# Kernel optimization log

Hardware: AMD Instinct MI355X
Metric: run time of the kernel (lower is better)

The kernel has to match this reference:

```python
import jax, jax.numpy as jnp
import numpy as np

B, T, D, H = 8, 4096, 256, 256

def setup_inputs() -> dict:
    key = jax.random.key(0)
    ks = jax.random.split(key, 6)
    scale = 1.0 / np.sqrt(D)
    return {
        "x": jax.random.normal(ks[0], (B, T, D), dtype=jnp.float32),
        "h0": jax.random.normal(ks[1], (B, H), dtype=jnp.float32),
        "Wz": jax.random.normal(ks[2], (H, D), dtype=jnp.float32) * scale,
        "bz": jax.random.normal(ks[3], (H,), dtype=jnp.float32) * scale,
        "Wh": jax.random.normal(ks[4], (H, D), dtype=jnp.float32) * scale,
        "bh": jax.random.normal(ks[5], (H,), dtype=jnp.float32) * scale,
    }

def reference(x, h0, Wz, bz, Wh, bh):
    # gate and update depend only on the input (minGRU): compute in one shot
    gate = jax.nn.sigmoid(jnp.einsum("btd,hd->bth", x, Wz) + bz)   # [B,T,H]
    update = jnp.einsum("btd,hd->bth", x, Wh) + bh                  # [B,T,H]

    def step(h, gu):
        g, u = gu
        h_new = (1.0 - g) * h + g * u
        return h_new, h_new

    # scan over time; xs laid out [T,B,H]
    _, hs = jax.lax.scan(step, h0, (jnp.swapaxes(gate, 0, 1), jnp.swapaxes(update, 0, 1)))
    return jnp.swapaxes(hs, 0, 1)  # [B,T,H]
```

## Files before the change

### kernel.cpp

```cpp
#include <hip/hip_runtime.h>
#include <hip/hip_fp16.h>


namespace {
constexpr int kB  = 8;
constexpr int kT  = 4096;
constexpr int kD  = 256;
constexpr int kH  = 256;
constexpr int kBT = kB * kT;

constexpr int TM  = 128;
constexpr int TH  = 64;
constexpr int BK  = 64;
constexpr int kNT = kT / TM;
constexpr int kNChain = kB * (kH / TH);
constexpr int EPS = 66;
}

typedef short s16x8 __attribute__((ext_vector_type(8)));
typedef short s16x4 __attribute__((ext_vector_type(4)));
typedef float f32x4 __attribute__((ext_vector_type(4)));

__device__ __forceinline__ short f2bf(float f) {
    union { float f; unsigned int u; } v; v.f = f;
    unsigned int r = v.u + 0x7fffu + ((v.u >> 16) & 1u);
    return (short)(r >> 16);
}

__device__ __forceinline__ unsigned int cvt_pk_bf16(float lo, float hi) {
    unsigned int r;
    asm("v_cvt_pk_bf16_f32 %0, %1, %2" : "=v"(r) : "v"(lo), "v"(hi));
    return r;
}

__device__ __forceinline__ void load_lds16(const void* g, void* l) {
    __builtin_amdgcn_global_load_lds(
        (const __attribute__((address_space(1))) void*)g,
        (__attribute__((address_space(3))) void*)l, 16, 0, 0);
}

__global__ __launch_bounds__(256)
void prep(const float* __restrict__ Wz,
          const float* __restrict__ Wh,
          unsigned short* __restrict__ wzb,
          unsigned short* __restrict__ whb,
          float4* __restrict__ aggz)
{
    constexpr int W4 = kH * kD / 4;
    const int i = blockIdx.x * 256 + threadIdx.x;

    if (i >= 2 * W4) {
        float4 z; z.x = 0.f; z.y = 0.f; z.z = 0.f; z.w = 0.f;
        aggz[i - 2 * W4] = z;
        return;
    }
    const float* src; unsigned short* dst; int j;
    if (i < W4) { src = Wz; dst = wzb; j = i; }
    else        { src = Wh; dst = whb; j = i - W4; }
    const float4 v = ((const float4*)src)[j];
    s16x4 p;
    p[0] = f2bf(v.x); p[1] = f2bf(v.y); p[2] = f2bf(v.z); p[3] = f2bf(v.w);
    ((s16x4*)dst)[j] = p;
}

__global__ __launch_bounds__(256, 4)
void gemm_scan_fused(const float* __restrict__ x,
                     const unsigned short* __restrict__ wzb,
                     const unsigned short* __restrict__ whb,
                     const float* __restrict__ bz,
                     const float* __restrict__ bh,
                     const float* __restrict__ h0,
                     unsigned long long* __restrict__ agg,
                     float* __restrict__ out)
{
    __shared__ __align__(16) unsigned char smem[36096];
    unsigned short* Xs  = (unsigned short*)smem;
    unsigned short* Wzs = Xs  + 128 * 64;
    unsigned short* Whs = Wzs + 64 * 64;
    __half* a_lds   = (__half*)smem;
    __half* b_lds   = a_lds + 128 * EPS;
    float2* sub_lds = (float2*)(smem + 33792);
    float*  hs_lds  = (float*)(smem + 35840);

    const int tid  = threadIdx.x;
    const int lane = tid & 63;
    const int wv   = tid >> 6;
    const int ln15 = lane & 15;
    const int quad = lane >> 4;
    const int wr0  = (wv & 1) * 64;
    const int wc0  = (wv >> 1) * 32;

    const int chain = blockIdx.x;
    const int t     = blockIdx.y;
    const int b     = chain >> 2;
    const int col0  = (chain & 3) * TH;
    const int row0  = b * kT + t * TM;

    const int srow = lane >> 3;
    const int swslot = (lane & 7) ^ srow;

    f32x4 accZ[4][2] = {};
    f32x4 accU[4][2] = {};

    for (int k0 = 0; k0 < kD; k0 += BK) {
        #pragma unroll
        for (int s = 0; s < 2; ++s) {
            const int seg = wv * 2 + s;
            const int m = seg * 8 + srow;
            load_lds16(wzb + (size_t)(col0 + m) * kD + k0 + swslot * 8,
                       Wzs + seg * 512);
            load_lds16(whb + (size_t)(col0 + m) * kD + k0 + swslot * 8,
                       Whs + seg * 512);
        }
        #pragma unroll
        for (int j = 0; j < 4; ++j) {
            const int bi  = j * 256 + tid;
            const int r   = bi >> 3;
            const int blk = bi & 7;
            const float* src = x + (size_t)(row0 + r) * kD + k0 + blk * 8;
            const float4 v0 = *(const float4*)src;
            const float4 v1 = *(const float4*)(src + 4);
            union { unsigned int u[4]; s16x8 v; } pk;
            pk.u[0] = cvt_pk_bf16(v0.x, v0.y);
            pk.u[1] = cvt_pk_bf16(v0.z, v0.w);
            pk.u[2] = cvt_pk_bf16(v1.x, v1.y);
            pk.u[3] = cvt_pk_bf16(v1.z, v1.w);
            *(s16x8*)&Xs[r * 64 + ((blk ^ (r & 7)) << 3)] = pk.v;
        }
        __syncthreads();

        #pragma unroll
        for (int kk = 0; kk < BK; kk += 32) {
            const int bblk = (kk >> 3) + quad;
            s16x8 af[4], bzf[2], buf[2];
            #pragma unroll
            for (int mt = 0; mt < 4; ++mt) {
                const int r = wr0 + mt * 16 + ln15;
                af[mt] = *(const s16x8*)&Xs[r * 64 + ((bblk ^ (r & 7)) << 3)];
            }
            #pragma unroll
            for (int nt = 0; nt < 2; ++nt) {
                const int rw = wc0 + nt * 16 + ln15;
                const int so = (bblk ^ (rw & 7)) << 3;
                bzf[nt] = *(const s16x8*)&Wzs[rw * 64 + so];
                buf[nt] = *(const s16x8*)&Whs[rw * 64 + so];
            }
            #pragma unroll
            for (int mt = 0; mt < 4; ++mt) {
                #pragma unroll
                for (int nt = 0; nt < 2; ++nt) {
                    accZ[mt][nt] = __builtin_amdgcn_mfma_f32_16x16x32_bf16(
                        af[mt], bzf[nt], accZ[mt][nt], 0, 0, 0);
                    accU[mt][nt] = __builtin_amdgcn_mfma_f32_16x16x32_bf16(
                        af[mt], buf[nt], accU[mt][nt], 0, 0, 0);
                }
            }
        }
        __syncthreads();
    }

    #pragma unroll
    for (int nt = 0; nt < 2; ++nt) {
        const int col = col0 + wc0 + nt * 16 + ln15;
        const int lc  = wc0 + nt * 16 + ln15;
        const float bzv = bz[col];
        const float bhv = bh[col];
        #pragma unroll
        for (int mt = 0; mt < 4; ++mt) {
            const int rb = wr0 + mt * 16 + quad * 4;
            #pragma unroll
            for (int r = 0; r < 4; ++r) {
                const float z = accZ[mt][nt][r] + bzv;
                const float g = 1.0f / (1.0f + __expf(-z));
                const float u = accU[mt][nt][r] + bhv;
                a_lds[(rb + r) * EPS + lc] = __float2half_rn(1.0f - g);
                b_lds[(rb + r) * EPS + lc] = __float2half_rn(g * u);
            }
        }
    }
    __syncthreads();

    const int s = tid >> 6;
    const int h = tid & 63;
    {
        float A = 1.0f, Bv = 0.0f;
        #pragma unroll 8
        for (int r = s * 32; r < s * 32 + 32; ++r) {
            const float a  = __half2float(a_lds[r * EPS + h]);
            const float bb = __half2float(b_lds[r * EPS + h]);
            Bv = fmaf(a, Bv, bb);
            A *= a;
        }
        float2 o; o.x = A; o.y = Bv;
        sub_lds[s * 64 + h] = o;
    }
    __syncthreads();

    if (tid < 64) {
        float A = 1.0f, Bv = 0.0f;
        #pragma unroll
        for (int s2 = 0; s2 < 4; ++s2) {
            const float2 g = sub_lds[s2 * 64 + tid];
            Bv = fmaf(g.x, Bv, g.y);
            A *= g.x;
        }
        union { float2 f; unsigned long long u; } pk;
        pk.f.x = A; pk.f.y = Bv;
        pk.u |= 1ull;
        __hip_atomic_store(&agg[(size_t)(chain * kNT + t) * 64 + tid], pk.u,
                           __ATOMIC_RELAXED, __HIP_MEMORY_SCOPE_AGENT);

        float hs = h0[(size_t)b * kH + col0 + tid];
        for (int j0 = 0; j0 < t; j0 += 8) {
            const int nb = (t - j0 < 8) ? (t - j0) : 8;
            unsigned long long u[8];
            #pragma unroll
            for (int q = 0; q < 8; ++q)
                if (q < nb)
                    u[q] = __hip_atomic_load(
                        &agg[(size_t)(chain * kNT + j0 + q) * 64 + tid],
                        __ATOMIC_RELAXED, __HIP_MEMORY_SCOPE_AGENT);
            #pragma unroll
            for (int q = 0; q < 8; ++q) {
                if (q < nb) {
                    while (u[q] == 0ull)
                        u[q] = __hip_atomic_load(
                            &agg[(size_t)(chain * kNT + j0 + q) * 64 + tid],
                            __ATOMIC_RELAXED, __HIP_MEMORY_SCOPE_AGENT);
                    union { unsigned long long u; float2 f; } qk; qk.u = u[q];
                    hs = fmaf(qk.f.x, hs, qk.f.y);
                }
            }
        }
        hs_lds[tid] = hs;
    }
    __syncthreads();

    {
        float hv = hs_lds[h];
        #pragma unroll
        for (int s2 = 0; s2 < s; ++s2) {
            const float2 g = sub_lds[s2 * 64 + h];
            hv = fmaf(g.x, hv, g.y);
        }
        #pragma unroll 8
        for (int r = 0; r < 32; ++r) {
            const int lr = s * 32 + r;
            const float a  = __half2float(a_lds[lr * EPS + h]);
            const float bb = __half2float(b_lds[lr * EPS + h]);
            hv = fmaf(a, hv, bb);
            __builtin_nontemporal_store(hv, &out[(size_t)(row0 + lr) * kH + col0 + h]);
        }
    }
}

extern "C" void kernel_launch(void* const* d_in, const int* in_sizes, int n_in,
                              void* d_out, int out_size, void* d_ws, size_t ws_size,
                              hipStream_t stream)
{
    const float* x  = (const float*)d_in[0];
    const float* h0 = (const float*)d_in[1];
    const float* Wz = (const float*)d_in[2];
    const float* bz = (const float*)d_in[3];
    const float* Wh = (const float*)d_in[4];
    const float* bh = (const float*)d_in[5];
    float* out = (float*)d_out;

    unsigned char* ws = (unsigned char*)d_ws;
    unsigned short* wzb = (unsigned short*)ws;   ws += (size_t)kH * kD * 2;
    unsigned short* whb = (unsigned short*)ws;   ws += (size_t)kH * kD * 2;
    unsigned long long* agg = (unsigned long long*)ws;

    constexpr int PREP_ITEMS = 2 * (kH * kD / 4)
                             + kNChain * kNT * TH * 8 / 16;
    prep<<<PREP_ITEMS / 256, 256, 0, stream>>>(
        Wz, Wh, wzb, whb, (float4*)agg);
    gemm_scan_fused<<<dim3(kNChain, kNT), 256, 0, stream>>>(
        x, wzb, whb, bz, bh, h0, agg, out);
}
```

Baseline: 116.0 us.

## Prefetch next x K-slice into registers during MFMA and raise MFMA wave priority

The GEMM K loop is restructured so the global loads of the next 64-wide x slice are issued into registers before the current slice's MFMAs run. The loaded values are converted to bf16 and written to LDS after the compute barrier, which hides global load latency behind matrix work. The MFMA block is also wrapped in s_setprio so waves doing math get issue priority. This costs extra VGPRs for the prefetch buffers, which may lower occupancy, and W loads still sit on the critical path between barriers.

```diff
diff --git a/kernel.cpp b/kernel.cpp
--- a/kernel.cpp
+++ b/kernel.cpp
@@ -99,35 +99,59 @@
     const int srow = lane >> 3;
     const int swslot = (lane & 7) ^ srow;
 
+    const int xr   = (tid >> 3) & 127;
+    float4 xv0[4], xv1[4];
+
     f32x4 accZ[4][2] = {};
     f32x4 accU[4][2] = {};
 
-    for (int k0 = 0; k0 < kD; k0 += BK) {
-        #pragma unroll
-        for (int s = 0; s < 2; ++s) {
-            const int seg = wv * 2 + s;
-            const int m = seg * 8 + srow;
-            load_lds16(wzb + (size_t)(col0 + m) * kD + k0 + swslot * 8,
-                       Wzs + seg * 512);
-            load_lds16(whb + (size_t)(col0 + m) * kD + k0 + swslot * 8,
-                       Whs + seg * 512);
-        }
-        #pragma unroll
-        for (int j = 0; j < 4; ++j) {
-            const int bi  = j * 256 + tid;
-            const int r   = bi >> 3;
-            const int blk = bi & 7;
-            const float* src = x + (size_t)(row0 + r) * kD + k0 + blk * 8;
-            const float4 v0 = *(const float4*)src;
-            const float4 v1 = *(const float4*)(src + 4);
-            union { unsigned int u[4]; s16x8 v; } pk;
-            pk.u[0] = cvt_pk_bf16(v0.x, v0.y);
-            pk.u[1] = cvt_pk_bf16(v0.z, v0.w);
-            pk.u[2] = cvt_pk_bf16(v1.x, v1.y);
-            pk.u[3] = cvt_pk_bf16(v1.z, v1.w);
-            *(s16x8*)&Xs[r * 64 + ((blk ^ (r & 7)) << 3)] = pk.v;
-        }
-        __syncthreads();
+    #pragma unroll
+    for (int j = 0; j < 4; ++j) {
+        const int bi  = j * 256 + tid;
+        const int r   = bi >> 3;
+        const int blk = bi & 7;
+        const float* src = x + (size_t)(row0 + r) * kD + blk * 8;
+        xv0[j] = *(const float4*)src;
+        xv1[j] = *(const float4*)(src + 4);
+    }
+    #pragma unroll
+    for (int s = 0; s < 2; ++s) {
+        const int seg = wv * 2 + s;
+        const int m = seg * 8 + srow;
+        load_lds16(wzb + (size_t)(col0 + m) * kD + swslot * 8,
+                   Wzs + seg * 512);
+        load_lds16(whb + (size_t)(col0 + m) * kD + swslot * 8,
+                   Whs + seg * 512);
+    }
+    #pragma unroll
+    for (int j = 0; j < 4; ++j) {
+        const int bi  = j * 256 + tid;
+        const int r   = bi >> 3;
+        const int blk = bi & 7;
+        union { unsigned int u[4]; s16x8 v; } pk;
+        pk.u[0] = cvt_pk_bf16(xv0[j].x, xv0[j].y);
+        pk.u[1] = cvt_pk_bf16(xv0[j].z, xv0[j].w);
+        pk.u[2] = cvt_pk_bf16(xv1[j].x, xv1[j].y);
+        pk.u[3] = cvt_pk_bf16(xv1[j].z, xv1[j].w);
+        *(s16x8*)&Xs[r * 64 + ((blk ^ (r & 7)) << 3)] = pk.v;
+    }
+    __syncthreads();
+
+    #pragma unroll
+    for (int k = 0; k < 4; ++k) {
+        const int k0n = (k + 1) * BK;
+        if (k < 3) {
+            #pragma unroll
+            for (int j = 0; j < 4; ++j) {
+                const int bi  = j * 256 + tid;
+                const int r   = bi >> 3;
+                const int blk = bi & 7;
+                const float* src = x + (size_t)(row0 + r) * kD + k0n + blk * 8;
+                xv0[j] = *(const float4*)src;
+                xv1[j] = *(const float4*)(src + 4);
+            }
+        }
+        __builtin_amdgcn_sched_barrier(0);
 
         #pragma unroll
         for (int kk = 0; kk < BK; kk += 32) {
@@ -145,6 +169,7 @@
                 bzf[nt] = *(const s16x8*)&Wzs[rw * 64 + so];
                 buf[nt] = *(const s16x8*)&Whs[rw * 64 + so];
             }
+            __builtin_amdgcn_s_setprio(1);
             #pragma unroll
             for (int mt = 0; mt < 4; ++mt) {
                 #pragma unroll
@@ -155,9 +180,36 @@
                         af[mt], buf[nt], accU[mt][nt], 0, 0, 0);
                 }
             }
+            __builtin_amdgcn_s_setprio(0);
         }
         __syncthreads();
-    }
+
+        if (k < 3) {
+            #pragma unroll
+            for (int s = 0; s < 2; ++s) {
+                const int seg = wv * 2 + s;
+                const int m = seg * 8 + srow;
+                load_lds16(wzb + (size_t)(col0 + m) * kD + k0n + swslot * 8,
+                           Wzs + seg * 512);
+                load_lds16(whb + (size_t)(col0 + m) * kD + k0n + swslot * 8,
+                           Whs + seg * 512);
+            }
+            #pragma unroll
+            for (int j = 0; j < 4; ++j) {
+                const int bi  = j * 256 + tid;
+                const int r   = bi >> 3;
+                const int blk = bi & 7;
+                union { unsigned int u[4]; s16x8 v; } pk;
+                pk.u[0] = cvt_pk_bf16(xv0[j].x, xv0[j].y);
+                pk.u[1] = cvt_pk_bf16(xv0[j].z, xv0[j].w);
+                pk.u[2] = cvt_pk_bf16(xv1[j].x, xv1[j].y);
+                pk.u[3] = cvt_pk_bf16(xv1[j].z, xv1[j].w);
+                *(s16x8*)&Xs[r * 64 + ((blk ^ (r & 7)) << 3)] = pk.v;
+            }
+            __syncthreads();
+        }
+    }
+    (void)xr;
 
     #pragma unroll
     for (int nt = 0; nt < 2; ++nt) {
```

Result: slower. 157.1 us (+35.4%).
